# Kernel tuning notes

Measured on AMD Instinct MI355X. Metric: run time of the kernel, lower is better.

The kernel has to match this reference:

```python
import jax, jax.numpy as jnp
import numpy as np

N_STATE = 1024
N_HEAD = 16
HEAD_DIM = N_STATE // N_HEAD
SEQLENS = [1024, 896, 768, 640, 512, 384, 896, 1024]  # sum = 6144
TOTAL = sum(SEQLENS)


def setup_inputs() -> dict:
    key = jax.random.key(0)
    ks = jax.random.split(key, 8)
    s = 0.02
    cu = jnp.asarray(np.concatenate([[0], np.cumsum(SEQLENS)]), dtype=jnp.int32)
    return {
        "x": jax.random.normal(ks[0], (TOTAL, N_STATE), jnp.float32),
        "cu_seqlens": cu,
        "Wq": jax.random.normal(ks[1], (N_STATE, N_STATE), jnp.float32) * s,
        "bq": jax.random.normal(ks[2], (N_STATE,), jnp.float32) * s,
        "Wk": jax.random.normal(ks[3], (N_STATE, N_STATE), jnp.float32) * s,
        "Wv": jax.random.normal(ks[4], (N_STATE, N_STATE), jnp.float32) * s,
        "bv": jax.random.normal(ks[5], (N_STATE,), jnp.float32) * s,
        "Wo": jax.random.normal(ks[6], (N_STATE, N_STATE), jnp.float32) * s,
        "bo": jax.random.normal(ks[7], (N_STATE,), jnp.float32) * s,
    }


def reference(x, cu_seqlens, Wq, bq, Wk, Wv, bv, Wo, bo):
    # cu_seqlens is a static (host) quantity in the original (used via .tolist())
    cu = np.asarray(jax.device_get(cu_seqlens))
    seqlens = cu[1:] - cu[:-1]
    B = len(seqlens)
    Lmax = int(seqlens.max())

    q = x @ Wq.T + bq              # [T, n_state]
    k = x @ Wk.T                   # key has no bias
    v = x @ Wv.T + bv

    # static pad/unpad index maps (honoring the ragged structure)
    ar = np.arange(Lmax)
    valid = ar[None, :] < seqlens[:, None]             # [B, Lmax]
    idx = np.where(valid, cu[:-1, None] + ar[None, :], 0)
    unpad_idx = np.nonzero(valid.reshape(-1))[0]       # flat positions of real tokens
    valid_j = jnp.asarray(valid)

    def pad(t):  # [T, n_state] -> [B, Lmax, H, D], zeros in padding
        p = jnp.where(valid_j[:, :, None], t[idx], 0.0)
        return p.reshape(B, Lmax, N_HEAD, HEAD_DIM)

    qp, kp, vp = pad(q), pad(k), pad(v)
    scale = HEAD_DIM ** -0.5
    # torch adds the bool mask (True->1.0) after masked_fill(mask==0, -max):
    # valid keys get +1.0 (softmax-invariant shift), invalid keys get -finfo.max
    big_neg = jnp.finfo(x.dtype).max
    add_mask = jnp.where(valid_j, 1.0, -big_neg)[:, None, None, :]  # [B,1,1,Lmax]

    scores = jnp.einsum("bqhd,bkhd->bhqk", qp, kp) * scale + add_mask
    weights = jax.nn.softmax(scores, axis=-1)
    ctx = jnp.einsum("bhqk,bkhd->bqhd", weights, vp)   # [B, Lmax, H, D]
    ctx_flat = ctx.reshape(B * Lmax, N_STATE)[unpad_idx]  # [T, n_state]
    return ctx_flat @ Wo.T + bo
```

## Files before the change

### kernel.cpp

```cpp
#include <hip/hip_runtime.h>

typedef unsigned short u16;
typedef unsigned int u32;
typedef __attribute__((ext_vector_type(8))) short bf16x8;
typedef __attribute__((ext_vector_type(4))) float f32x4;

#define MFMA_BF16(a, b, c) __builtin_amdgcn_mfma_f32_16x16x32_bf16((a), (b), (c), 0, 0, 0)

#define QSCALE 0.18033688011112042f

__device__ __forceinline__ u16 f2bf(float f) {
    union { float f; unsigned u; } v; v.f = f;
    return (u16)((v.u + 0x7FFFu + ((v.u >> 16) & 1u)) >> 16);
}

__device__ __forceinline__ u32 pkbf(float a, float b) {
    union { float f; unsigned u; } x, y; x.f = a; y.f = b;
    return ((x.u + 0x8000u) >> 16) | ((y.u + 0x8000u) & 0xFFFF0000u);
}

__device__ __forceinline__ void async16(const void* g, void* l) {
    __builtin_amdgcn_global_load_lds(
        (const __attribute__((address_space(1))) void*)g,
        (__attribute__((address_space(3))) void*)l, 16, 0, 0);
}

__global__ __launch_bounds__(256) void cvt_all(
    const float* __restrict__ x, const float* __restrict__ Wq, const float* __restrict__ Wk,
    const float* __restrict__ Wv, const float* __restrict__ Wo,
    u16* __restrict__ xb, u16* __restrict__ Wqb, u16* __restrict__ Wkb,
    u16* __restrict__ Wvb, u16* __restrict__ Wob) {
    int b = blockIdx.x;
    const float* src; u16* dst; int base;
    if (b < 6144)      { src = x;  dst = xb;  base = b; }
    else if (b < 7168) { src = Wq; dst = Wqb; base = b - 6144; }
    else if (b < 8192) { src = Wk; dst = Wkb; base = b - 7168; }
    else if (b < 9216) { src = Wv; dst = Wvb; base = b - 8192; }
    else               { src = Wo; dst = Wob; base = b - 9216; }
    int i = base * 256 + threadIdx.x;
    float4 v = ((const float4*)src)[i];
    unsigned long long pk = (unsigned long long)f2bf(v.x)
                          | ((unsigned long long)f2bf(v.y) << 16)
                          | ((unsigned long long)f2bf(v.z) << 32)
                          | ((unsigned long long)f2bf(v.w) << 48);
    *(unsigned long long*)(dst + (size_t)i * 4) = pk;
}

__global__ __launch_bounds__(256) void gemm_qkv(
    const u16* __restrict__ xb,
    const u16* __restrict__ Wqb, const u16* __restrict__ Wkb, const u16* __restrict__ Wvb,
    const float* __restrict__ bq, const float* __restrict__ bv,
    u16* __restrict__ qb, u16* __restrict__ kb, u16* __restrict__ vbT) {
    __shared__ __align__(16) u16 As[2][128 * 64];
    __shared__ __align__(16) u16 Bs[2][128 * 64];
    const int tid = threadIdx.x;

    const int fid = blockIdx.x;
    const int xcd = fid & 7;
    const int slot = fid >> 3;
    const int mloc = slot % 6;
    const int nidx = slot / 6;
    const int m0 = (xcd * 6 + mloc) << 7;
    const int buf = nidx >> 3;
    const int n0 = (nidx & 7) << 7;
    const u16* __restrict__ W = (buf == 0) ? Wqb : (buf == 1) ? Wkb : Wvb;

    const int rr = tid >> 3;
    const int cg = tid & 7;
    const int wv = tid >> 6, lane = tid & 63, g = lane >> 4, c = lane & 15;
    const int wm = (wv & 1) << 6, wn = (wv >> 1) << 6;

    const int sw = (cg ^ (rr & 7)) << 3;
    const u16* gA[4]; const u16* gB[4];
#pragma unroll
    for (int r = 0; r < 4; ++r) {
        gA[r] = xb + (size_t)(m0 + (r << 5) + rr) * 1024 + sw;
        gB[r] = W + (size_t)(n0 + (r << 5) + rr) * 1024 + sw;
    }

    f32x4 zero = {0.f, 0.f, 0.f, 0.f};
    f32x4 acc[4][4];
#pragma unroll
    for (int i = 0; i < 4; ++i)
#pragma unroll
        for (int j = 0; j < 4; ++j) acc[i][j] = zero;

#pragma unroll
    for (int r = 0; r < 4; ++r) {
        async16(gA[r], &As[0][(r << 11) + tid * 8]);
        async16(gB[r], &Bs[0][(r << 11) + tid * 8]);
    }
    __syncthreads();

    for (int kt = 0; kt < 16; ++kt) {
        const int cur = kt & 1;
        if (kt < 15) {
            const int k0 = (kt + 1) << 6;
#pragma unroll
            for (int r = 0; r < 4; ++r) {
                async16(gA[r] + k0, &As[cur ^ 1][(r << 11) + tid * 8]);
                async16(gB[r] + k0, &Bs[cur ^ 1][(r << 11) + tid * 8]);
            }
        }
#pragma unroll
        for (int ks = 0; ks < 2; ++ks) {
            bf16x8 af[4], bb[4];
#pragma unroll
            for (int i = 0; i < 4; ++i) {
                int ra = wm + (i << 4) + c;
                af[i] = *(const bf16x8*)(&As[cur][ra * 64 + ((((ks << 2) + g) ^ (ra & 7)) << 3)]);
                int rb = wn + (i << 4) + c;
                bb[i] = *(const bf16x8*)(&Bs[cur][rb * 64 + ((((ks << 2) + g) ^ (rb & 7)) << 3)]);
            }
#pragma unroll
            for (int i = 0; i < 4; ++i)
#pragma unroll
                for (int j = 0; j < 4; ++j) acc[i][j] = MFMA_BF16(af[i], bb[j], acc[i][j]);
        }
        __syncthreads();
    }

    if (buf == 0) {
#pragma unroll
        for (int j = 0; j < 4; ++j) {
            int col = n0 + wn + (j << 4) + c;
            float bias = bq[col];
#pragma unroll
            for (int i = 0; i < 4; ++i) {
                int rowb = m0 + wm + (i << 4) + (g << 2);
#pragma unroll
                for (int r = 0; r < 4; ++r)
                    qb[(size_t)(rowb + r) * 1024 + col] = f2bf((acc[i][j][r] + bias) * QSCALE);
            }
        }
    } else if (buf == 1) {
#pragma unroll
        for (int j = 0; j < 4; ++j) {
            int col = n0 + wn + (j << 4) + c;
#pragma unroll
            for (int i = 0; i < 4; ++i) {
                int rowb = m0 + wm + (i << 4) + (g << 2);
#pragma unroll
                for (int r = 0; r < 4; ++r)
                    kb[(size_t)(rowb + r) * 1024 + col] = f2bf(acc[i][j][r]);
            }
        }
    } else {
#pragma unroll
        for (int j = 0; j < 4; ++j) {
            int col = n0 + wn + (j << 4) + c;
            float bias = bv[col];
#pragma unroll
            for (int i = 0; i < 4; ++i) {
                int trow = m0 + wm + (i << 4) + (g << 2);
                unsigned long long pk =
                      (unsigned long long)f2bf(acc[i][j][0] + bias)
                    | ((unsigned long long)f2bf(acc[i][j][1] + bias) << 16)
                    | ((unsigned long long)f2bf(acc[i][j][2] + bias) << 32)
                    | ((unsigned long long)f2bf(acc[i][j][3] + bias) << 48);
                *(unsigned long long*)(vbT + (size_t)col * 6144 + trow) = pk;
            }
        }
    }
}

__global__ __launch_bounds__(256) void gemm_out(
    const u16* __restrict__ ctxb, const u16* __restrict__ Wob,
    const float* __restrict__ bo, float* __restrict__ out) {
    __shared__ __align__(16) u16 As[2][64 * 64];
    __shared__ __align__(16) u16 Bs[2][64 * 64];
    const int tid = threadIdx.x;

    const int fid = blockIdx.x;
    const int xcd = fid & 7;
    const int slot = fid >> 3;
    const int mloc = slot % 12;
    const int nidx = slot / 12;
    const int m0 = (xcd * 12 + mloc) << 6;
    const int n0 = nidx << 6;

    const int rr = tid >> 3, cg = tid & 7;
    const int wv = tid >> 6, lane = tid & 63, g = lane >> 4, c = lane & 15;
    const int wm = (wv & 1) << 5, wn = (wv >> 1) << 5;

    const int sw = (cg ^ (rr & 7)) << 3;
    const u16* gA[2]; const u16* gB[2];
#pragma unroll
    for (int r = 0; r < 2; ++r) {
        gA[r] = ctxb + (size_t)(m0 + (r << 5) + rr) * 1024 + sw;
        gB[r] = Wob + (size_t)(n0 + (r << 5) + rr) * 1024 + sw;
    }

    f32x4 zero = {0.f, 0.f, 0.f, 0.f};
    f32x4 acc[2][2];
#pragma unroll
    for (int i = 0; i < 2; ++i)
#pragma unroll
        for (int j = 0; j < 2; ++j) acc[i][j] = zero;

#pragma unroll
    for (int r = 0; r < 2; ++r) {
        async16(gA[r], &As[0][(r << 11) + tid * 8]);
        async16(gB[r], &Bs[0][(r << 11) + tid * 8]);
    }
    __syncthreads();

    for (int kt = 0; kt < 16; ++kt) {
        const int cur = kt & 1;
        if (kt < 15) {
            const int k0 = (kt + 1) << 6;
#pragma unroll
            for (int r = 0; r < 2; ++r) {
                async16(gA[r] + k0, &As[cur ^ 1][(r << 11) + tid * 8]);
                async16(gB[r] + k0, &Bs[cur ^ 1][(r << 11) + tid * 8]);
            }
        }
#pragma unroll
        for (int ks = 0; ks < 2; ++ks) {
            bf16x8 af[2], bb[2];
#pragma unroll
            for (int i = 0; i < 2; ++i) {
                int ra = wm + (i << 4) + c;
                af[i] = *(const bf16x8*)(&As[cur][ra * 64 + ((((ks << 2) + g) ^ (ra & 7)) << 3)]);
                int rb = wn + (i << 4) + c;
                bb[i] = *(const bf16x8*)(&Bs[cur][rb * 64 + ((((ks << 2) + g) ^ (rb & 7)) << 3)]);
            }
#pragma unroll
            for (int i = 0; i < 2; ++i)
#pragma unroll
                for (int j = 0; j < 2; ++j) acc[i][j] = MFMA_BF16(af[i], bb[j], acc[i][j]);
        }
        __syncthreads();
    }

#pragma unroll
    for (int j = 0; j < 2; ++j) {
        int col = n0 + wn + (j << 4) + c;
        float bias = bo[col];
#pragma unroll
        for (int i = 0; i < 2; ++i) {
            int rowb = m0 + wm + (i << 4) + (g << 2);
#pragma unroll
            for (int r = 0; r < 4; ++r)
                out[(size_t)(rowb + r) * 1024 + col] = acc[i][j][r] + bias;
        }
    }
}

__global__ __launch_bounds__(256) void attn_kernel(const u16* __restrict__ qb,
                                                   const u16* __restrict__ kb,
                                                   const u16* __restrict__ vbT,
                                                   u16* __restrict__ ctxb) {
    __shared__ __align__(16) u16 Ks[2][128 * 64];
    __shared__ __align__(16) u16 Vs[2][64 * 128];
    __shared__ __align__(16) u16 Ps[4 * 2048];

    const int tid = threadIdx.x;
    const int fid = blockIdx.x;
    const int xcd = fid & 7;
    const int slot = fid >> 3;
    const int h = (xcd << 1) + (slot >= 96 ? 1 : 0);
    const int q0 = (slot % 96) << 6;

    const int cuv[9] = {0, 1024, 1920, 2688, 3328, 3840, 4224, 5120, 6144};
    int s0 = 0, e0 = 6144;
#pragma unroll
    for (int i = 1; i < 8; ++i) {
        if (q0 >= cuv[i]) s0 = cuv[i];
        if (q0 < cuv[i] && cuv[i] < e0) e0 = cuv[i];
    }
    const int ntiles = (e0 - s0) >> 7;

    const int wv = tid >> 6, lane = tid & 63, g = lane >> 4, c = lane & 15;
    const int wrow = wv << 4;

    auto stageKV = [&](int kv0, int b) {
        const int rr = tid >> 3, cg = tid & 7;
#pragma unroll
        for (int r = 0; r < 4; ++r) {
            int row = (r << 5) + rr;
            async16(kb + (size_t)(kv0 + row) * 1024 + (h << 6) + ((cg ^ (row & 7)) << 3),
                    &Ks[b][(r << 11) + tid * 8]);
        }
        const int rr2 = tid >> 4, cg2 = tid & 15;
#pragma unroll
        for (int r = 0; r < 4; ++r) {
            int row = (r << 4) + rr2;
            async16(vbT + (size_t)((h << 6) + row) * 6144 + kv0 + ((cg2 ^ (row & 15)) << 3),
                    &Vs[b][(r << 11) + tid * 8]);
        }
    };

    {
        const int rr = tid >> 3, cg = tid & 7;
#pragma unroll
        for (int r = 0; r < 2; ++r) {
            int row = (r << 5) + rr;
            async16(qb + (size_t)(q0 + row) * 1024 + (h << 6) + ((cg ^ (row & 7)) << 3),
                    Ps + (r << 11) + tid * 8);
        }
        stageKV(s0, 0);
    }
    __syncthreads();

    bf16x8 qf[2];
#pragma unroll
    for (int ks = 0; ks < 2; ++ks) {
        int row = wrow + c;
        qf[ks] = *(const bf16x8*)(Ps + row * 64 + ((((ks << 2) + g) ^ (row & 7)) << 3));
    }
    __syncthreads();

    float m_run = -1e30f, l_run = 0.f;
    f32x4 zero = {0.f, 0.f, 0.f, 0.f};
    f32x4 oacc[4];
#pragma unroll
    for (int nt = 0; nt < 4; ++nt) oacc[nt] = zero;

    const int pbase = (wv << 11) + c * 128;
    const int c7 = c & 7;

    for (int kt = 0; kt < ntiles; ++kt) {
        const int cur = kt & 1;
        if (kt + 1 < ntiles) stageKV(s0 + ((kt + 1) << 7), cur ^ 1);

        f32x4 st[8];
#pragma unroll
        for (int mt = 0; mt < 8; ++mt) st[mt] = zero;
#pragma unroll
        for (int mt = 0; mt < 8; ++mt) {
            int row = (mt << 4) + c;
            int sw = row & 7;
#pragma unroll
            for (int ks = 0; ks < 2; ++ks) {
                bf16x8 kf = *(const bf16x8*)(&Ks[cur][row * 64 + ((((ks << 2) + g) ^ sw) << 3)]);
                st[mt] = MFMA_BF16(kf, qf[ks], st[mt]);
            }
        }

        float mx = st[0][0];
#pragma unroll
        for (int mt = 0; mt < 8; ++mt)
#pragma unroll
            for (int r = 0; r < 4; ++r) mx = fmaxf(mx, st[mt][r]);
        mx = fmaxf(mx, __shfl_xor(mx, 16, 64));
        mx = fmaxf(mx, __shfl_xor(mx, 32, 64));
        float mnew = fmaxf(m_run, mx);
        float alpha = exp2f(m_run - mnew);
        m_run = mnew;

        float rsum = 0.f;
#pragma unroll
        for (int mt = 0; mt < 8; ++mt) {
            float p0 = exp2f(st[mt][0] - mnew);
            float p1 = exp2f(st[mt][1] - mnew);
            float p2 = exp2f(st[mt][2] - mnew);
            float p3 = exp2f(st[mt][3] - mnew);
            rsum += (p0 + p1) + (p2 + p3);
            int ph = ((mt << 2) + g) ^ (c7 << 1);
            *(uint2*)(Ps + pbase + (ph << 2)) = make_uint2(pkbf(p0, p1), pkbf(p2, p3));
        }
        rsum += __shfl_xor(rsum, 16, 64);
        rsum += __shfl_xor(rsum, 32, 64);
        l_run = l_run * alpha + rsum;

        float al[4];
#pragma unroll
        for (int r = 0; r < 4; ++r) al[r] = __shfl(alpha, (g << 2) + r, 16);
#pragma unroll
        for (int nt = 0; nt < 4; ++nt)
#pragma unroll
            for (int r = 0; r < 4; ++r) oacc[nt][r] *= al[r];

#pragma unroll
        for (int ks = 0; ks < 4; ++ks) {
            int pg = ((ks << 2) + g) ^ c7;
            bf16x8 pf = *(const bf16x8*)(Ps + pbase + (pg << 3));
#pragma unroll
            for (int nt = 0; nt < 4; ++nt) {
                int vrow = (nt << 4) + c;
                bf16x8 vf = *(const bf16x8*)(&Vs[cur][vrow * 128 + ((((ks << 2) + g) ^ (vrow & 15)) << 3)]);
                oacc[nt] = MFMA_BF16(pf, vf, oacc[nt]);
            }
        }
        __syncthreads();
    }

    float inv = 1.0f / l_run;
    float invr[4];
#pragma unroll
    for (int r = 0; r < 4; ++r) invr[r] = __shfl(inv, (g << 2) + r, 16);
#pragma unroll
    for (int r = 0; r < 4; ++r) {
        size_t rowoff = (size_t)(q0 + wrow + (g << 2) + r) * 1024 + (h << 6);
#pragma unroll
        for (int nt = 0; nt < 4; ++nt)
            ctxb[rowoff + (nt << 4) + c] = f2bf(oacc[nt][r] * invr[r]);
    }
}

extern "C" void kernel_launch(void* const* d_in, const int* in_sizes, int n_in,
                              void* d_out, int out_size, void* d_ws, size_t ws_size,
                              hipStream_t stream) {
    const float* x  = (const float*)d_in[0];
    const float* Wq = (const float*)d_in[2];
    const float* bq = (const float*)d_in[3];
    const float* Wk = (const float*)d_in[4];
    const float* Wv = (const float*)d_in[5];
    const float* bv = (const float*)d_in[6];
    const float* Wo = (const float*)d_in[7];
    const float* bo = (const float*)d_in[8];
    float* out = (float*)d_out;

    u16* ws = (u16*)d_ws;
    u16* xb   = ws;
    u16* Wqb  = xb + 6291456;
    u16* Wkb  = Wqb + 1048576;
    u16* Wvb  = Wkb + 1048576;
    u16* Wob  = Wvb + 1048576;
    u16* qb   = Wob + 1048576;
    u16* kb   = qb + 6291456;
    u16* vbT  = kb + 6291456;
    u16* ctxb = xb;

    cvt_all<<<10240, 256, 0, stream>>>(x, Wq, Wk, Wv, Wo, xb, Wqb, Wkb, Wvb, Wob);
    gemm_qkv<<<1152, 256, 0, stream>>>(xb, Wqb, Wkb, Wvb, bq, bv, qb, kb, vbT);
    attn_kernel<<<1536, 256, 0, stream>>>(qb, kb, vbT, ctxb);
    gemm_out<<<1536, 256, 0, stream>>>(ctxb, Wob, bo, out);
}
```

Before: 250.8 us.

## Keep GEMM tile loads in flight across barriers; single-buffer attention KV

The projection and output GEMMs now prefetch two K-tiles ahead. They use explicit s_waitcnt vmcnt counts and raw s_barrier in place of __syncthreads, so the next tile's async global-to-LDS loads stay in flight across the barrier instead of being drained at the end of every iteration. The attention kernel drops KV double buffering and loads each K/V tile synchronously before computing on it. That cuts its LDS footprint, which may allow more resident blocks per CU, but it gives up load/compute overlap inside a block. The hand-written waitcnt and barrier sequencing is fragile if the number of loads per stage ever changes.

```diff
diff --git a/kernel.cpp b/kernel.cpp
--- a/kernel.cpp
+++ b/kernel.cpp
@@ -90,18 +90,17 @@
         async16(gA[r], &As[0][(r << 11) + tid * 8]);
         async16(gB[r], &Bs[0][(r << 11) + tid * 8]);
     }
-    __syncthreads();
+#pragma unroll
+    for (int r = 0; r < 4; ++r) {
+        async16(gA[r] + 64, &As[1][(r << 11) + tid * 8]);
+        async16(gB[r] + 64, &Bs[1][(r << 11) + tid * 8]);
+    }
+    asm volatile("s_waitcnt vmcnt(8)" ::: "memory");
+    __builtin_amdgcn_s_barrier();
+    __builtin_amdgcn_sched_barrier(0);
 
     for (int kt = 0; kt < 16; ++kt) {
         const int cur = kt & 1;
-        if (kt < 15) {
-            const int k0 = (kt + 1) << 6;
-#pragma unroll
-            for (int r = 0; r < 4; ++r) {
-                async16(gA[r] + k0, &As[cur ^ 1][(r << 11) + tid * 8]);
-                async16(gB[r] + k0, &Bs[cur ^ 1][(r << 11) + tid * 8]);
-            }
-        }
 #pragma unroll
         for (int ks = 0; ks < 2; ++ks) {
             bf16x8 af[4], bb[4];
@@ -117,7 +116,22 @@
 #pragma unroll
                 for (int j = 0; j < 4; ++j) acc[i][j] = MFMA_BF16(af[i], bb[j], acc[i][j]);
         }
-        __syncthreads();
+        if (kt == 15) break;
+        __builtin_amdgcn_sched_barrier(0);
+        __builtin_amdgcn_s_barrier();
+        if (kt < 14) {
+            const int k0 = (kt + 2) << 6;
+#pragma unroll
+            for (int r = 0; r < 4; ++r) {
+                async16(gA[r] + k0, &As[cur][(r << 11) + tid * 8]);
+                async16(gB[r] + k0, &Bs[cur][(r << 11) + tid * 8]);
+            }
+            asm volatile("s_waitcnt vmcnt(8)" ::: "memory");
+        } else {
+            asm volatile("s_waitcnt vmcnt(0)" ::: "memory");
+        }
+        __builtin_amdgcn_s_barrier();
+        __builtin_amdgcn_sched_barrier(0);
     }
 
     if (buf == 0) {
@@ -203,18 +217,17 @@
         async16(gA[r], &As[0][(r << 11) + tid * 8]);
         async16(gB[r], &Bs[0][(r << 11) + tid * 8]);
     }
-    __syncthreads();
+#pragma unroll
+    for (int r = 0; r < 2; ++r) {
+        async16(gA[r] + 64, &As[1][(r << 11) + tid * 8]);
+        async16(gB[r] + 64, &Bs[1][(r << 11) + tid * 8]);
+    }
+    asm volatile("s_waitcnt vmcnt(4)" ::: "memory");
+    __builtin_amdgcn_s_barrier();
+    __builtin_amdgcn_sched_barrier(0);
 
     for (int kt = 0; kt < 16; ++kt) {
         const int cur = kt & 1;
-        if (kt < 15) {
-            const int k0 = (kt + 1) << 6;
-#pragma unroll
-            for (int r = 0; r < 2; ++r) {
-                async16(gA[r] + k0, &As[cur ^ 1][(r << 11) + tid * 8]);
-                async16(gB[r] + k0, &Bs[cur ^ 1][(r << 11) + tid * 8]);
-            }
-        }
 #pragma unroll
         for (int ks = 0; ks < 2; ++ks) {
             bf16x8 af[2], bb[2];
@@ -230,7 +243,22 @@
 #pragma unroll
                 for (int j = 0; j < 2; ++j) acc[i][j] = MFMA_BF16(af[i], bb[j], acc[i][j]);
         }
-        __syncthreads();
+        if (kt == 15) break;
+        __builtin_amdgcn_sched_barrier(0);
+        __builtin_amdgcn_s_barrier();
+        if (kt < 14) {
+            const int k0 = (kt + 2) << 6;
+#pragma unroll
+            for (int r = 0; r < 2; ++r) {
+                async16(gA[r] + k0, &As[cur][(r << 11) + tid * 8]);
+                async16(gB[r] + k0, &Bs[cur][(r << 11) + tid * 8]);
+            }
+            asm volatile("s_waitcnt vmcnt(4)" ::: "memory");
+        } else {
+            asm volatile("s_waitcnt vmcnt(0)" ::: "memory");
+        }
+        __builtin_amdgcn_s_barrier();
+        __builtin_amdgcn_sched_barrier(0);
     }
 
 #pragma unroll
@@ -251,8 +279,8 @@
                                                    const u16* __restrict__ kb,
                                                    const u16* __restrict__ vbT,
                                                    u16* __restrict__ ctxb) {
-    __shared__ __align__(16) u16 Ks[2][128 * 64];
-    __shared__ __align__(16) u16 Vs[2][64 * 128];
+    __shared__ __align__(16) u16 Ks[128 * 64];
+    __shared__ __align__(16) u16 Vs[64 * 128];
     __shared__ __align__(16) u16 Ps[4 * 2048];
 
     const int tid = threadIdx.x;
@@ -274,23 +302,6 @@
     const int wv = tid >> 6, lane = tid & 63, g = lane >> 4, c = lane & 15;
     const int wrow = wv << 4;
 
-    auto stageKV = [&](int kv0, int b) {
-        const int rr = tid >> 3, cg = tid & 7;
-#pragma unroll
-        for (int r = 0; r < 4; ++r) {
-            int row = (r << 5) + rr;
-            async16(kb + (size_t)(kv0 + row) * 1024 + (h << 6) + ((cg ^ (row & 7)) << 3),
-                    &Ks[b][(r << 11) + tid * 8]);
-        }
-        const int rr2 = tid >> 4, cg2 = tid & 15;
-#pragma unroll
-        for (int r = 0; r < 4; ++r) {
-            int row = (r << 4) + rr2;
-            async16(vbT + (size_t)((h << 6) + row) * 6144 + kv0 + ((cg2 ^ (row & 15)) << 3),
-                    &Vs[b][(r << 11) + tid * 8]);
-        }
-    };
-
     {
         const int rr = tid >> 3, cg = tid & 7;
 #pragma unroll
@@ -299,7 +310,6 @@
             async16(qb + (size_t)(q0 + row) * 1024 + (h << 6) + ((cg ^ (row & 7)) << 3),
                     Ps + (r << 11) + tid * 8);
         }
-        stageKV(s0, 0);
     }
     __syncthreads();
 
@@ -309,7 +319,6 @@
         int row = wrow + c;
         qf[ks] = *(const bf16x8*)(Ps + row * 64 + ((((ks << 2) + g) ^ (row & 7)) << 3));
     }
-    __syncthreads();
 
     float m_run = -1e30f, l_run = 0.f;
     f32x4 zero = {0.f, 0.f, 0.f, 0.f};
@@ -321,8 +330,25 @@
     const int c7 = c & 7;
 
     for (int kt = 0; kt < ntiles; ++kt) {
-        const int cur = kt & 1;
-        if (kt + 1 < ntiles) stageKV(s0 + ((kt + 1) << 7), cur ^ 1);
+        const int kv0 = s0 + (kt << 7);
+        __syncthreads();
+        {
+            const int rr = tid >> 3, cg = tid & 7;
+#pragma unroll
+            for (int r = 0; r < 4; ++r) {
+                int row = (r << 5) + rr;
+                async16(kb + (size_t)(kv0 + row) * 1024 + (h << 6) + ((cg ^ (row & 7)) << 3),
+                        Ks + (r << 11) + tid * 8);
+            }
+            const int rr2 = tid >> 4, cg2 = tid & 15;
+#pragma unroll
+            for (int r = 0; r < 4; ++r) {
+                int row = (r << 4) + rr2;
+                async16(vbT + (size_t)((h << 6) + row) * 6144 + kv0 + ((cg2 ^ (row & 15)) << 3),
+                        Vs + (r << 11) + tid * 8);
+            }
+        }
+        __syncthreads();
 
         f32x4 st[8];
 #pragma unroll
@@ -333,7 +359,7 @@
             int sw = row & 7;
 #pragma unroll
             for (int ks = 0; ks < 2; ++ks) {
-                bf16x8 kf = *(const bf16x8*)(&Ks[cur][row * 64 + ((((ks << 2) + g) ^ sw) << 3)]);
+                bf16x8 kf = *(const bf16x8*)(&Ks[row * 64 + ((((ks << 2) + g) ^ sw) << 3)]);
                 st[mt] = MFMA_BF16(kf, qf[ks], st[mt]);
             }
         }
@@ -379,11 +405,10 @@
 #pragma unroll
             for (int nt = 0; nt < 4; ++nt) {
                 int vrow = (nt << 4) + c;
-                bf16x8 vf = *(const bf16x8*)(&Vs[cur][vrow * 128 + ((((ks << 2) + g) ^ (vrow & 15)) << 3)]);
+                bf16x8 vf = *(const bf16x8*)(&Vs[vrow * 128 + ((((ks << 2) + g) ^ (vrow & 15)) << 3)]);
                 oacc[nt] = MFMA_BF16(pf, vf, oacc[nt]);
             }
         }
-        __syncthreads();
     }
 
     float inv = 1.0f / l_run;
```

New measurement: 228.5 us. 8.9% less time.
